# Performance work log

Measured on AMD Instinct MI355X. Metric: run time of the kernel, lower is better.

## Reference

```python
import jax, jax.numpy as jnp
import numpy as np

B, F, H, K, E = 512, 1280, 2560, 8, 9  # batch, feat_dim, 2*feat_dim, branching, n_internal
# Tree: root=node 0 (expert 0); level-1 nodes 1..8 (experts 1..8); level-2 leaves 9..72.

def setup_inputs() -> dict:
    key = jax.random.key(0)
    k0, k1, k2, k3, k4 = jax.random.split(key, 5)
    x = jax.random.normal(k0, (B, F), dtype=jnp.float32)
    W1 = jax.random.normal(k1, (E, F, H), dtype=jnp.float32) / np.sqrt(F)
    b1 = jnp.zeros((E, H), dtype=jnp.float32)
    W2 = jax.random.normal(k2, (E, H, K), dtype=jnp.float32) / np.sqrt(H)
    b2 = jnp.zeros((E, K), dtype=jnp.float32)
    return {"x": x, "W1": W1, "b1": b1, "W2": W2, "b2": b2}

def reference(x, W1, b1, W2, b2):
    # Batched experts: Linear(F->H) -> ReLU -> Linear(H->K), softmax over children.
    h = jax.nn.relu(jnp.einsum('bf,efh->ebh', x, W1) + b1[:, None, :])  # [E,B,H]
    logits = jnp.einsum('ebh,ehk->ebk', h, W2) + b2[:, None, :]          # [E,B,K]
    probs = jax.nn.softmax(logits, axis=-1)                              # [E,B,K]
    # Path products root->node for every node (matches leaf_probs in torch code).
    p0 = jnp.ones((1, x.shape[0]), dtype=x.dtype)        # root: prob 1        [1,B]
    p1 = probs[0].T                                       # nodes 1..8          [K,B]
    # leaves 9..72: parent of node n is 1+(n-9)//K, child index (n-9)%K
    p2 = (p1[:, None, :] * jnp.transpose(probs[1:E], (0, 2, 1))).reshape(K * K, -1)  # [64,B]
    leaf_probs = jnp.concatenate([p0, p1, p2], axis=0).T  # [B, 73]
    return leaf_probs, logits
```

## Files before the change

kernel.cpp:

```cpp
#include <hip/hip_runtime.h>

#define TB 512
#define TF 1280
#define TH 2560
#define TK 8
#define TE 9
#define SLOT 8192
#define BUFSZ 32768

typedef unsigned short ushortT;
typedef unsigned long long u64;
typedef __attribute__((ext_vector_type(8))) short short8;
typedef __attribute__((ext_vector_type(4))) short short4v;
typedef __attribute__((ext_vector_type(4))) float floatx4;

__device__ __forceinline__ unsigned short f2bf(float f) {
  union { float f; unsigned u; } v; v.f = f;
  unsigned r = v.u + 0x7fffu + ((v.u >> 16) & 1u);
  return (unsigned short)(r >> 16);
}

__device__ __forceinline__ unsigned pk2(float a, float b) {
  union { float f; unsigned u; } ua, ub; ua.f = a; ub.f = b;
  unsigned ra = ua.u + 0x7fffu + ((ua.u >> 16) & 1u);
  unsigned rb = ub.u + 0x7fffu + ((ub.u >> 16) & 1u);
  return __builtin_amdgcn_perm(rb, ra, 0x07060302);
}

__device__ __forceinline__ void gl_lds16(const void* g, void* l) {
  __builtin_amdgcn_global_load_lds(
      (const __attribute__((address_space(1))) unsigned*)g,
      (__attribute__((address_space(3))) unsigned*)l, 16, 0, 0);
}

__device__ __forceinline__ int swz(int o) { return o ^ (((o >> 7) & 7) << 4); }

__global__ __launch_bounds__(256) void prep_all(
    const float* __restrict__ x, const float* __restrict__ W1,
    const float* __restrict__ W2,
    char* __restrict__ Apk, ushortT* __restrict__ W2t, char* __restrict__ W1p,
    float* __restrict__ lacc) {
  const int b = blockIdx.x;
  const int t = threadIdx.x;
  if (b < 7200) {
    __shared__ ushortT Ts[128 * 40];
    const int khalf = b & 1;
    const int kt = (b >> 1) % 20;
    const int nt = ((b >> 1) / 20) % 20;
    const int e = b / 800;
    const int kbase = kt * 64 + khalf * 32;
    const int nbase = nt * 128;
    const int kr = t >> 5, n4 = (t & 31) * 4;
#pragma unroll
    for (int kk = 0; kk < 4; ++kk) {
      const int k2 = kk * 8 + kr;
      floatx4 v = *(const floatx4*)(W1 + ((long)e * TF + kbase + k2) * TH + nbase + n4);
#pragma unroll
      for (int i = 0; i < 4; ++i) Ts[(n4 + i) * 40 + k2] = f2bf(v[i]);
    }
    __syncthreads();
    char* dstbase = W1p + (long)b * SLOT;
#pragma unroll
    for (int p = 0; p < 2; ++p) {
      const int op = (p * 256 + t) * 16;
      const int o = swz(op);
      const int r = o >> 6, k2c = (o & 63) >> 1;
      short8 v = *(const short8*)&Ts[r * 40 + k2c];
      *(short8*)(dstbase + op) = v;
    }
  } else if (b < 7520) {
    const int i = (b - 7200) * 256 + t;
    const int cc = i & 511, slot = i >> 9;
    const int khalf = slot & 1;
    const int kt = (slot >> 1) % 20;
    const int mt = slot / 40;
    const int op = cc * 16;
    const int o = swz(op);
    const int r = o >> 6, k2 = (o & 63) >> 1;
    const float* src = x + (long)(mt * 128 + r) * TF + kt * 64 + khalf * 32 + k2;
    floatx4 v0 = *(const floatx4*)(src);
    floatx4 v1 = *(const floatx4*)(src + 4);
    u64 q0 = (u64)pk2(v0.x, v0.y) | ((u64)pk2(v0.z, v0.w) << 32);
    u64 q1 = (u64)pk2(v1.x, v1.y) | ((u64)pk2(v1.z, v1.w) << 32);
    *(ulonglong2*)(Apk + (long)i * 16) = make_ulonglong2(q0, q1);
  } else if (b < 8240) {
    const int o = (b - 7520) * 256 + t;
    if (o < TE * TK * TH) {
      const int hcol = o % TH;
      const int rest = o / TH;
      const int n = rest & 7;
      const int e = rest >> 3;
      W2t[(long)(e * TK + n) * TH + hcol] = f2bf(W2[((long)e * TH + hcol) * TK + n]);
    }
  } else {
    const int i = ((b - 8240) * 256 + t) * 4;
    if (i < TE * TB * TK)
      *(floatx4*)(lacc + i) = (floatx4){0.f, 0.f, 0.f, 0.f};
  }
}

__global__ __launch_bounds__(256) void prepass(
    const float* __restrict__ x, const float* __restrict__ W2,
    u64* __restrict__ xq, ushortT* __restrict__ W2t) {
  const int i = blockIdx.x * 256 + threadIdx.x;
  if (i < 320 * 512) {
    const int kq = i >> 9, m = i & 511;
    floatx4 v = *(const floatx4*)(x + (long)m * TF + kq * 4);
    xq[i] = (u64)pk2(v.x, v.y) | ((u64)pk2(v.z, v.w) << 32);
  } else {
    const int o = i - 320 * 512;
    if (o < TE * TK * TH) {
      const int hcol = o % TH;
      const int rest = o / TH;
      const int n = rest & 7;
      const int e = rest >> 3;
      W2t[(long)(e * TK + n) * TH + hcol] = f2bf(W2[((long)e * TH + hcol) * TK + n]);
    }
  }
}

__global__ __launch_bounds__(256, 2) void gemm1_fused(
    const char* __restrict__ Apk, const char* __restrict__ Bpk,
    const float* __restrict__ b1, const ushortT* __restrict__ W2t,
    float* __restrict__ lacc) {
  __shared__ __align__(16) char lds[65536];
  const int t = threadIdx.x;
  const int lane = t & 63, w = t >> 6;
  const int wm = w >> 1, wn = w & 1;
  const int lm = lane & 15, lq = lane >> 4;
  const int bid0 = blockIdx.x;
  const int bs = (bid0 & 7) * 90 + (bid0 >> 3);
  const int mt = bs & 3;
  const int ct = bs >> 2;
  const int nt = ct % 20, e = ct / 20;

  const char* Ab = Apk + (long)mt * 40 * SLOT;
  const char* Bb = Bpk + (long)((e * 20 + nt) * 40) * SLOT;

  int oA[4], oB[4];
#pragma unroll
  for (int mi = 0; mi < 4; ++mi)
    oA[mi] = swz((wm * 64 + mi * 16 + lm) * 64 + lq * 16);
#pragma unroll
  for (int ni = 0; ni < 4; ++ni)
    oB[ni] = swz((wn * 64 + ni * 16 + lm) * 64 + lq * 16);

  auto STAGE = [&](int tile, int half) {
    if (tile >= 20) return;
    const char* src = (half & 1)
        ? Bb + (long)(tile * 2 + (half >> 1)) * SLOT
        : Ab + (long)(tile * 2 + (half >> 1)) * SLOT;
    char* dst = lds + (tile & 1) * BUFSZ + half * SLOT + w * 1024;
    gl_lds16(src + t * 16, dst);
    gl_lds16(src + 4096 + t * 16, dst + 4096);
  };

  floatx4 acc[4][4];
#pragma unroll
  for (int i = 0; i < 4; ++i)
#pragma unroll
    for (int j = 0; j < 4; ++j) acc[i][j] = (floatx4){0.f, 0.f, 0.f, 0.f};

  STAGE(0, 0); STAGE(0, 1); STAGE(0, 2); STAGE(0, 3);
  STAGE(1, 0); STAGE(1, 1); STAGE(1, 2);
  asm volatile("s_waitcnt vmcnt(6)" ::: "memory");
  __builtin_amdgcn_s_barrier();

  for (int j = 0; j < 20; ++j) {
    const char* buf = lds + (j & 1) * BUFSZ;
    short8 af[4], bfA, bfB;
#pragma unroll
    for (int mi = 0; mi < 4; ++mi)
      af[mi] = *(const short8*)(buf + 0 * SLOT + oA[mi]);
    bfA = *(const short8*)(buf + 1 * SLOT + oB[0]);
    bfB = *(const short8*)(buf + 1 * SLOT + oB[1]);
    STAGE(j + 1, 3);
    __builtin_amdgcn_s_barrier();
    asm volatile("s_waitcnt lgkmcnt(0)" ::: "memory");
    __builtin_amdgcn_sched_barrier(0);
    __builtin_amdgcn_s_setprio(1);
#pragma unroll
    for (int mi = 0; mi < 4; ++mi) {
      acc[mi][0] = __builtin_amdgcn_mfma_f32_16x16x32_bf16(af[mi], bfA, acc[mi][0], 0, 0, 0);
      acc[mi][1] = __builtin_amdgcn_mfma_f32_16x16x32_bf16(af[mi], bfB, acc[mi][1], 0, 0, 0);
    }
    __builtin_amdgcn_s_setprio(0);
    __builtin_amdgcn_s_barrier();
    bfA = *(const short8*)(buf + 1 * SLOT + oB[2]);
    bfB = *(const short8*)(buf + 1 * SLOT + oB[3]);
    STAGE(j + 2, 0);
    __builtin_amdgcn_s_barrier();
    asm volatile("s_waitcnt lgkmcnt(0)" ::: "memory");
    __builtin_amdgcn_sched_barrier(0);
    __builtin_amdgcn_s_setprio(1);
#pragma unroll
    for (int mi = 0; mi < 4; ++mi) {
      acc[mi][2] = __builtin_amdgcn_mfma_f32_16x16x32_bf16(af[mi], bfA, acc[mi][2], 0, 0, 0);
      acc[mi][3] = __builtin_amdgcn_mfma_f32_16x16x32_bf16(af[mi], bfB, acc[mi][3], 0, 0, 0);
    }
    __builtin_amdgcn_s_setprio(0);
    __builtin_amdgcn_s_barrier();
#pragma unroll
    for (int mi = 0; mi < 4; ++mi)
      af[mi] = *(const short8*)(buf + 2 * SLOT + oA[mi]);
    bfA = *(const short8*)(buf + 3 * SLOT + oB[0]);
    bfB = *(const short8*)(buf + 3 * SLOT + oB[1]);
    STAGE(j + 2, 1);
    __builtin_amdgcn_s_barrier();
    asm volatile("s_waitcnt lgkmcnt(0)" ::: "memory");
    __builtin_amdgcn_sched_barrier(0);
    __builtin_amdgcn_s_setprio(1);
#pragma unroll
    for (int mi = 0; mi < 4; ++mi) {
      acc[mi][0] = __builtin_amdgcn_mfma_f32_16x16x32_bf16(af[mi], bfA, acc[mi][0], 0, 0, 0);
      acc[mi][1] = __builtin_amdgcn_mfma_f32_16x16x32_bf16(af[mi], bfB, acc[mi][1], 0, 0, 0);
    }
    __builtin_amdgcn_s_setprio(0);
    __builtin_amdgcn_s_barrier();
    bfA = *(const short8*)(buf + 3 * SLOT + oB[2]);
    bfB = *(const short8*)(buf + 3 * SLOT + oB[3]);
    STAGE(j + 2, 2);
    if (j >= 18) {
      asm volatile("s_waitcnt vmcnt(0)" ::: "memory");
    } else {
      asm volatile("s_waitcnt vmcnt(6)" ::: "memory");
    }
    __builtin_amdgcn_s_barrier();
    asm volatile("s_waitcnt lgkmcnt(0)" ::: "memory");
    __builtin_amdgcn_sched_barrier(0);
    __builtin_amdgcn_s_setprio(1);
#pragma unroll
    for (int mi = 0; mi < 4; ++mi) {
      acc[mi][2] = __builtin_amdgcn_mfma_f32_16x16x32_bf16(af[mi], bfA, acc[mi][2], 0, 0, 0);
      acc[mi][3] = __builtin_amdgcn_mfma_f32_16x16x32_bf16(af[mi], bfB, acc[mi][3], 0, 0, 0);
    }
    __builtin_amdgcn_s_setprio(0);
    __builtin_amdgcn_s_barrier();
  }

  short8 bq[4];
  {
    const ushortT* wp = W2t + ((long)(e * TK + (lm < 8 ? lm : 0))) * TH
                        + nt * 128 + lq * 8;
#pragma unroll
    for (int kk = 0; kk < 4; ++kk) bq[kk] = *(const short8*)(wp + kk * 32);
    if (lm >= 8) {
#pragma unroll
      for (int kk = 0; kk < 4; ++kk) bq[kk] = (short8)0;
    }
  }

#pragma unroll
  for (int ni = 0; ni < 4; ++ni) {
    const int lcol = wn * 64 + ni * 16 + lm;
    const float bias = b1[e * TH + nt * 128 + lcol];
#pragma unroll
    for (int mi = 0; mi < 4; ++mi) {
      const int lr0 = wm * 64 + mi * 16 + lq * 4;
      floatx4 c = acc[mi][ni];
#pragma unroll
      for (int r = 0; r < 4; ++r) {
        float v = c[r] + bias;
        v = v > 0.f ? v : 0.f;
        const int lrow = lr0 + r;
        const int o = (lrow * 256 + lcol * 2) ^ ((lrow & 7) << 4);
        *(ushortT*)(lds + o) = f2bf(v);
      }
    }
  }
  __syncthreads();

  floatx4 acc2[2];
  acc2[0] = (floatx4){0.f, 0.f, 0.f, 0.f};
  acc2[1] = (floatx4){0.f, 0.f, 0.f, 0.f};
#pragma unroll
  for (int rt = 0; rt < 2; ++rt) {
    const int row = (w * 2 + rt) * 16 + lm;
    const int rowb = row * 256;
    const int sx = (row & 7) << 4;
#pragma unroll
    for (int kk = 0; kk < 4; ++kk) {
      short8 a = *(const short8*)(lds + ((rowb + kk * 64 + lq * 16) ^ sx));
      acc2[rt] = __builtin_amdgcn_mfma_f32_16x16x32_bf16(a, bq[kk], acc2[rt], 0, 0, 0);
    }
  }
  if (lm < 8) {
#pragma unroll
    for (int rt = 0; rt < 2; ++rt) {
      const int growb = mt * 128 + (w * 2 + rt) * 16 + lq * 4;
#pragma unroll
      for (int r = 0; r < 4; ++r)
        atomicAdd(&lacc[((long)e * TB + growb + r) * TK + lm], acc2[rt][r]);
    }
  }
}

__global__ __launch_bounds__(256) void finish(
    const float* __restrict__ lacc, const float* __restrict__ b2,
    float* __restrict__ out, float* __restrict__ logits_out) {
  const int b = blockIdx.x * 256 + threadIdx.x;
  if (b >= TB) return;
  float pr[TE][TK];
#pragma unroll
  for (int e = 0; e < TE; ++e) {
    float lg[TK];
    float mx = -1e30f;
#pragma unroll
    for (int k = 0; k < TK; ++k) {
      lg[k] = lacc[((long)e * TB + b) * TK + k] + b2[e * TK + k];
      logits_out[((long)e * TB + b) * TK + k] = lg[k];
      mx = fmaxf(mx, lg[k]);
    }
    float sm = 0.f;
#pragma unroll
    for (int k = 0; k < TK; ++k) { pr[e][k] = __expf(lg[k] - mx); sm += pr[e][k]; }
    const float inv = 1.f / sm;
#pragma unroll
    for (int k = 0; k < TK; ++k) pr[e][k] *= inv;
  }
  float* op = out + (long)b * 73;
  op[0] = 1.0f;
#pragma unroll
  for (int i = 0; i < 8; ++i) op[1 + i] = pr[0][i];
#pragma unroll
  for (int i = 0; i < 8; ++i)
#pragma unroll
    for (int j = 0; j < 8; ++j) op[9 + i * 8 + j] = pr[0][i] * pr[1 + i][j];
}

__global__ __launch_bounds__(256) void gemm1_fb(
    const float* __restrict__ x, const float* __restrict__ W1,
    const float* __restrict__ b1, ushortT* __restrict__ h) {
  __shared__ __align__(16) ushortT As[128 * 40];
  __shared__ __align__(16) ushortT Bs[128 * 40];
  const int t = threadIdx.x;
  const int tileN = blockIdx.x;
  const int e = tileN / 20;
  const int hbase = (tileN % 20) * 128;
  const int m0 = blockIdx.y * 128;
  const int lane = t & 63, w = t >> 6;
  const int wm = w & 1, wn = w >> 1;
  const int lm = lane & 15, lq = lane >> 4;
  const int lk = lq * 8;
  floatx4 acc[4][4];
#pragma unroll
  for (int i = 0; i < 4; ++i)
#pragma unroll
    for (int j = 0; j < 4; ++j) acc[i][j] = (floatx4){0.f, 0.f, 0.f, 0.f};
  const float* wp = W1 + (long)e * TF * TH + hbase;
  const int cA = (t & 7) * 4;
  const int mA = t >> 3;
  const int nB = t & 127;
  const int gB = t >> 7;
  for (int kt = 0; kt < TF / 32; ++kt) {
    const int k0 = kt * 32;
    if (kt) __syncthreads();
#pragma unroll
    for (int i = 0; i < 4; ++i) {
      const int m = mA + 32 * i;
      floatx4 v = *(const floatx4*)(x + (long)(m0 + m) * TF + k0 + cA);
      short4v s; s.x = f2bf(v.x); s.y = f2bf(v.y); s.z = f2bf(v.z); s.w = f2bf(v.w);
      *(short4v*)&As[m * 40 + cA] = s;
    }
    {
      const float* bp = wp + (long)k0 * TH + nB;
#pragma unroll
      for (int q = 0; q < 4; ++q) {
        const int k4 = gB * 16 + q * 4;
        float f0 = bp[(long)(k4 + 0) * TH];
        float f1 = bp[(long)(k4 + 1) * TH];
        float f2 = bp[(long)(k4 + 2) * TH];
        float f3 = bp[(long)(k4 + 3) * TH];
        short4v s; s.x = f2bf(f0); s.y = f2bf(f1); s.z = f2bf(f2); s.w = f2bf(f3);
        *(short4v*)&Bs[nB * 40 + k4] = s;
      }
    }
    __syncthreads();
    short8 af[4], bfr[4];
#pragma unroll
    for (int mg = 0; mg < 4; ++mg)
      af[mg] = *(const short8*)&As[(wm * 64 + mg * 16 + lm) * 40 + lk];
#pragma unroll
    for (int ng = 0; ng < 4; ++ng)
      bfr[ng] = *(const short8*)&Bs[(wn * 64 + ng * 16 + lm) * 40 + lk];
#pragma unroll
    for (int mg = 0; mg < 4; ++mg)
#pragma unroll
      for (int ng = 0; ng < 4; ++ng)
        acc[mg][ng] = __builtin_amdgcn_mfma_f32_16x16x32_bf16(af[mg], bfr[ng], acc[mg][ng], 0, 0, 0);
  }
#pragma unroll
  for (int mg = 0; mg < 4; ++mg) {
    const int row = m0 + wm * 64 + mg * 16 + lq * 4;
#pragma unroll
    for (int ng = 0; ng < 4; ++ng) {
      const int col = hbase + wn * 64 + ng * 16 + lm;
      const float bias = b1[e * TH + col];
      floatx4 c = acc[mg][ng];
#pragma unroll
      for (int r = 0; r < 4; ++r) {
        float v = c[r] + bias;
        v = v > 0.f ? v : 0.f;
        h[((long)e * TB + row + r) * TH + col] = f2bf(v);
      }
    }
  }
}

__global__ __launch_bounds__(512) void gemm2_softmax(
    const ushortT* __restrict__ h, const ushortT* __restrict__ W2t,
    const float* __restrict__ b2, float* __restrict__ logits_out,
    float* __restrict__ probs) {
  __shared__ float Ls[8][16][8];
  const int t = threadIdx.x;
  const int lane = t & 63, w = t >> 6;
  const int e = blockIdx.x >> 5;
  const int r0 = (blockIdx.x & 31) * 16;
  const int lm = lane & 15, lq = lane >> 4;

  const ushortT* hp = h + ((long)(e * TB + r0 + lm)) * TH + w * 320 + lq * 8;
  const int bn = lm < 8 ? lm : 7;
  const ushortT* wp = W2t + ((long)(e * TK + bn)) * TH + w * 320 + lq * 8;

  floatx4 acc = (floatx4){0.f, 0.f, 0.f, 0.f};
#pragma unroll
  for (int kt = 0; kt < 10; ++kt) {
    short8 a = *(const short8*)(hp + kt * 32);
    short8 b = *(const short8*)(wp + kt * 32);
    acc = __builtin_amdgcn_mfma_f32_16x16x32_bf16(a, b, acc, 0, 0, 0);
  }
  if (lm < 8) {
#pragma unroll
    for (int r = 0; r < 4; ++r) Ls[w][lq * 4 + r][lm] = acc[r];
  }
  __syncthreads();
  if (w == 0 && lm < 8) {
    const float bias = b2[e * TK + lm];
#pragma unroll
    for (int r = 0; r < 4; ++r) {
      const int row = lq * 4 + r;
      float v = Ls[0][row][lm] + Ls[1][row][lm] + Ls[2][row][lm] + Ls[3][row][lm]
              + Ls[4][row][lm] + Ls[5][row][lm] + Ls[6][row][lm] + Ls[7][row][lm]
              + bias;
      float mx = v;
      mx = fmaxf(mx, __shfl_xor(mx, 1, 64));
      mx = fmaxf(mx, __shfl_xor(mx, 2, 64));
      mx = fmaxf(mx, __shfl_xor(mx, 4, 64));
      float ex = __expf(v - mx);
      float sm = ex;
      sm += __shfl_xor(sm, 1, 64);
      sm += __shfl_xor(sm, 2, 64);
      sm += __shfl_xor(sm, 4, 64);
      const long idx = ((long)e * TB + r0 + row) * TK + lm;
      logits_out[idx] = v;
      probs[idx] = ex / sm;
    }
  }
}

__global__ __launch_bounds__(256) void leafk(const float* __restrict__ probs,
                                             float* __restrict__ out) {
  const int idx = blockIdx.x * 256 + threadIdx.x;
  if (idx >= TB * 73) return;
  const int b = idx / 73, c = idx % 73;
  float v;
  if (c == 0) {
    v = 1.0f;
  } else if (c < 9) {
    v = probs[(long)b * TK + (c - 1)];
  } else {
    const int i = (c - 9) >> 3, j = (c - 9) & 7;
    v = probs[(long)b * TK + i] * probs[((long)(1 + i) * TB + b) * TK + j];
  }
  out[idx] = v;
}

extern "C" void kernel_launch(void* const* d_in, const int* in_sizes, int n_in,
                              void* d_out, int out_size, void* d_ws, size_t ws_size,
                              hipStream_t stream) {
  const float* x  = (const float*)d_in[0];
  const float* W1 = (const float*)d_in[1];
  const float* b1 = (const float*)d_in[2];
  const float* W2 = (const float*)d_in[3];
  const float* b2 = (const float*)d_in[4];
  float* out = (float*)d_out;

  ushortT* h     = (ushortT*)d_ws;
  float*   lacc  = (float*)((char*)d_ws + 23592960);
  char*    Apk   = (char*)d_ws + 23740416;
  ushortT* W2t   = (ushortT*)((char*)d_ws + 25051136);
  char*    W1p   = (char*)d_ws + 25419776;
  const size_t NEED = 25419776 + 58982400;
  float* logits_out = out + TB * 73;

  if (ws_size >= NEED) {
    prep_all<<<8276, 256, 0, stream>>>(x, W1, W2, Apk, W2t, W1p, lacc);
    gemm1_fused<<<720, 256, 0, stream>>>(Apk, W1p, b1, W2t, lacc);
    finish<<<2, 256, 0, stream>>>(lacc, b2, out, logits_out);
  } else {
    prepass<<<1360, 256, 0, stream>>>(x, W2, (u64*)Apk, W2t);
    gemm1_fb<<<dim3(180, 4), 256, 0, stream>>>(x, W1, b1, h);
    gemm2_softmax<<<TE * 32, 512, 0, stream>>>(h, W2t, b2, logits_out, lacc);
    leafk<<<(TB * 73 + 255) / 256, 256, 0, stream>>>(lacc, out);
  }
}
```

Baseline: 227.3 us.

## Halve LDS tile buffers and simplify pipeline to raise gemm1 occupancy

Replaces the four-phase fine-grained staging loop (two 32 KB buffers, two tiles in flight) with a simple double buffer holding one K-slice of A and B per 16 KB buffer, iterating 40 times instead of 20. LDS drops from 64 KB to 32 KB and launch bounds rise to four blocks per CU, so more waves can hide latency. In exchange each iteration issues only one tile ahead and waits on vmcnt(0) at every step, which weakens the prefetch depth and intra-block overlap.

```diff
diff --git a/kernel.cpp b/kernel.cpp
--- a/kernel.cpp
+++ b/kernel.cpp
@@ -6,7 +6,7 @@
 #define TK 8
 #define TE 9
 #define SLOT 8192
-#define BUFSZ 32768
+#define BUFSZ 16384
 
 typedef unsigned short ushortT;
 typedef unsigned long long u64;
@@ -119,11 +119,11 @@
   }
 }
 
-__global__ __launch_bounds__(256, 2) void gemm1_fused(
+__global__ __launch_bounds__(256, 4) void gemm1_fused(
     const char* __restrict__ Apk, const char* __restrict__ Bpk,
     const float* __restrict__ b1, const ushortT* __restrict__ W2t,
     float* __restrict__ lacc) {
-  __shared__ __align__(16) char lds[65536];
+  __shared__ __align__(16) char lds[32768];
   const int t = threadIdx.x;
   const int lane = t & 63, w = t >> 6;
   const int wm = w >> 1, wn = w & 1;
@@ -145,14 +145,15 @@
   for (int ni = 0; ni < 4; ++ni)
     oB[ni] = swz((wn * 64 + ni * 16 + lm) * 64 + lq * 16);
 
-  auto STAGE = [&](int tile, int half) {
-    if (tile >= 20) return;
-    const char* src = (half & 1)
-        ? Bb + (long)(tile * 2 + (half >> 1)) * SLOT
-        : Ab + (long)(tile * 2 + (half >> 1)) * SLOT;
-    char* dst = lds + (tile & 1) * BUFSZ + half * SLOT + w * 1024;
-    gl_lds16(src + t * 16, dst);
-    gl_lds16(src + 4096 + t * 16, dst + 4096);
+  auto STAGE = [&](int tile) {
+    if (tile >= 40) return;
+    char* dst = lds + (tile & 1) * BUFSZ + w * 1024;
+    const char* sa = Ab + (long)tile * SLOT;
+    const char* sb = Bb + (long)tile * SLOT;
+    gl_lds16(sa + t * 16, dst);
+    gl_lds16(sa + 4096 + t * 16, dst + 4096);
+    gl_lds16(sb + t * 16, dst + 8192);
+    gl_lds16(sb + 4096 + t * 16, dst + 12288);
   };
 
   floatx4 acc[4][4];
@@ -161,80 +162,30 @@
 #pragma unroll
     for (int j = 0; j < 4; ++j) acc[i][j] = (floatx4){0.f, 0.f, 0.f, 0.f};
 
-  STAGE(0, 0); STAGE(0, 1); STAGE(0, 2); STAGE(0, 3);
-  STAGE(1, 0); STAGE(1, 1); STAGE(1, 2);
-  asm volatile("s_waitcnt vmcnt(6)" ::: "memory");
+  STAGE(0);
+  asm volatile("s_waitcnt vmcnt(0)" ::: "memory");
   __builtin_amdgcn_s_barrier();
 
-  for (int j = 0; j < 20; ++j) {
+  for (int j = 0; j < 40; ++j) {
     const char* buf = lds + (j & 1) * BUFSZ;
-    short8 af[4], bfA, bfB;
+    STAGE(j + 1);
+    short8 af[4], bfr[4];
 #pragma unroll
     for (int mi = 0; mi < 4; ++mi)
-      af[mi] = *(const short8*)(buf + 0 * SLOT + oA[mi]);
-    bfA = *(const short8*)(buf + 1 * SLOT + oB[0]);
-    bfB = *(const short8*)(buf + 1 * SLOT + oB[1]);
-    STAGE(j + 1, 3);
-    __builtin_amdgcn_s_barrier();
+      af[mi] = *(const short8*)(buf + oA[mi]);
+#pragma unroll
+    for (int ni = 0; ni < 4; ++ni)
+      bfr[ni] = *(const short8*)(buf + 8192 + oB[ni]);
     asm volatile("s_waitcnt lgkmcnt(0)" ::: "memory");
     __builtin_amdgcn_sched_barrier(0);
     __builtin_amdgcn_s_setprio(1);
 #pragma unroll
-    for (int mi = 0; mi < 4; ++mi) {
-      acc[mi][0] = __builtin_amdgcn_mfma_f32_16x16x32_bf16(af[mi], bfA, acc[mi][0], 0, 0, 0);
-      acc[mi][1] = __builtin_amdgcn_mfma_f32_16x16x32_bf16(af[mi], bfB, acc[mi][1], 0, 0, 0);
-    }
+    for (int mi = 0; mi < 4; ++mi)
+#pragma unroll
+      for (int ni = 0; ni < 4; ++ni)
+        acc[mi][ni] = __builtin_amdgcn_mfma_f32_16x16x32_bf16(af[mi], bfr[ni], acc[mi][ni], 0, 0, 0);
     __builtin_amdgcn_s_setprio(0);
-    __builtin_amdgcn_s_barrier();
-    bfA = *(const short8*)(buf + 1 * SLOT + oB[2]);
-    bfB = *(const short8*)(buf + 1 * SLOT + oB[3]);
-    STAGE(j + 2, 0);
-    __builtin_amdgcn_s_barrier();
-    asm volatile("s_waitcnt lgkmcnt(0)" ::: "memory");
-    __builtin_amdgcn_sched_barrier(0);
-    __builtin_amdgcn_s_setprio(1);
-#pragma unroll
-    for (int mi = 0; mi < 4; ++mi) {
-      acc[mi][2] = __builtin_amdgcn_mfma_f32_16x16x32_bf16(af[mi], bfA, acc[mi][2], 0, 0, 0);
-      acc[mi][3] = __builtin_amdgcn_mfma_f32_16x16x32_bf16(af[mi], bfB, acc[mi][3], 0, 0, 0);
-    }
-    __builtin_amdgcn_s_setprio(0);
-    __builtin_amdgcn_s_barrier();
-#pragma unroll
-    for (int mi = 0; mi < 4; ++mi)
-      af[mi] = *(const short8*)(buf + 2 * SLOT + oA[mi]);
-    bfA = *(const short8*)(buf + 3 * SLOT + oB[0]);
-    bfB = *(const short8*)(buf + 3 * SLOT + oB[1]);
-    STAGE(j + 2, 1);
-    __builtin_amdgcn_s_barrier();
-    asm volatile("s_waitcnt lgkmcnt(0)" ::: "memory");
-    __builtin_amdgcn_sched_barrier(0);
-    __builtin_amdgcn_s_setprio(1);
-#pragma unroll
-    for (int mi = 0; mi < 4; ++mi) {
-      acc[mi][0] = __builtin_amdgcn_mfma_f32_16x16x32_bf16(af[mi], bfA, acc[mi][0], 0, 0, 0);
-      acc[mi][1] = __builtin_amdgcn_mfma_f32_16x16x32_bf16(af[mi], bfB, acc[mi][1], 0, 0, 0);
-    }
-    __builtin_amdgcn_s_setprio(0);
-    __builtin_amdgcn_s_barrier();
-    bfA = *(const short8*)(buf + 3 * SLOT + oB[2]);
-    bfB = *(const short8*)(buf + 3 * SLOT + oB[3]);
-    STAGE(j + 2, 2);
-    if (j >= 18) {
-      asm volatile("s_waitcnt vmcnt(0)" ::: "memory");
-    } else {
-      asm volatile("s_waitcnt vmcnt(6)" ::: "memory");
-    }
-    __builtin_amdgcn_s_barrier();
-    asm volatile("s_waitcnt lgkmcnt(0)" ::: "memory");
-    __builtin_amdgcn_sched_barrier(0);
-    __builtin_amdgcn_s_setprio(1);
-#pragma unroll
-    for (int mi = 0; mi < 4; ++mi) {
-      acc[mi][2] = __builtin_amdgcn_mfma_f32_16x16x32_bf16(af[mi], bfA, acc[mi][2], 0, 0, 0);
-      acc[mi][3] = __builtin_amdgcn_mfma_f32_16x16x32_bf16(af[mi], bfB, acc[mi][3], 0, 0, 0);
-    }
-    __builtin_amdgcn_s_setprio(0);
+    asm volatile("s_waitcnt vmcnt(0)" ::: "memory");
     __builtin_amdgcn_s_barrier();
   }
 
```

Measured after the change: 228.5 us. No clear change (+0.5%).
